# Kernel optimization log

Hardware: AMD Instinct MI355X
Metric: run time of the kernel (lower is better)

## Reference

```python
import jax, jax.numpy as jnp
import numpy as np
import math

B, S, HID = 2, 2048, 512
NH, NKV, HD = 8, 2, 256
ROT = 64          # partial_rotary_factor 0.25 * head_dim 256
ROPE_THETA = 10000000.0
EPS = 1e-6


def _rms_norm(x, w):
    # zero-centered RMSNorm: x / rms * (1 + w)
    rms = jnp.sqrt(jnp.mean(x * x, axis=-1, keepdims=True) + EPS)
    return x / rms * (1.0 + w)


def _partial_rope(x, cos, sin):
    # x: [B,S,H,HD]; cos/sin: [S, ROT//2]
    xr = x[..., :ROT].reshape(*x.shape[:-1], ROT // 2, 2)
    a, b = xr[..., 0], xr[..., 1]
    c = cos[None, :, None, :]
    s = sin[None, :, None, :]
    rot = jnp.stack([a * c - b * s, a * s + b * c], axis=-1).reshape(*x.shape[:-1], ROT)
    return jnp.concatenate([rot, x[..., ROT:]], axis=-1)


def setup_inputs() -> dict:
    key = jax.random.key(0)
    ks = jax.random.split(key, 6)
    x = jax.random.normal(ks[0], (B, S, HID), dtype=jnp.float32)
    # real RoPE frequencies
    inv_freq = 1.0 / (ROPE_THETA ** (np.arange(0, ROT, 2, dtype=np.float32) / ROT))
    t = np.arange(S, dtype=np.float32)
    angles = np.outer(t, inv_freq)  # [S, ROT//2]
    cos = jnp.asarray(np.cos(angles), dtype=jnp.float32)
    sin = jnp.asarray(np.sin(angles), dtype=jnp.float32)
    # additive causal mask [S,S]
    mask = jnp.where(jnp.tril(jnp.ones((S, S), dtype=bool)), 0.0, -1e9).astype(jnp.float32)
    sc = 0.02
    wq = jax.random.normal(ks[1], (HID, NH * HD), dtype=jnp.float32) * sc
    wk = jax.random.normal(ks[2], (HID, NKV * HD), dtype=jnp.float32) * sc
    wv = jax.random.normal(ks[3], (HID, NKV * HD), dtype=jnp.float32) * sc
    wo = jax.random.normal(ks[4], (NH * HD, HID), dtype=jnp.float32) * sc
    q_norm_w = jnp.zeros((HD,), dtype=jnp.float32)
    k_norm_w = jnp.zeros((HD,), dtype=jnp.float32)
    return {"x": x, "cos": cos, "sin": sin, "mask": mask,
            "wq": wq, "wk": wk, "wv": wv, "wo": wo,
            "q_norm_w": q_norm_w, "k_norm_w": k_norm_w}


def reference(x, cos, sin, mask, wq, wk, wv, wo, q_norm_w, k_norm_w):
    b, s, _ = x.shape
    groups = NH // NKV
    q = (x @ wq).reshape(b, s, NH, HD)
    k = (x @ wk).reshape(b, s, NKV, HD)
    v = (x @ wv).reshape(b, s, NKV, HD)
    q = _partial_rope(_rms_norm(q, q_norm_w), cos, sin)
    k = _partial_rope(_rms_norm(k, k_norm_w), cos, sin)
    # GQA: broadcast kv heads to NH
    k = jnp.repeat(k, groups, axis=2)  # [b,s,NH,HD]
    v = jnp.repeat(v, groups, axis=2)
    scale = math.sqrt(HD)
    scores = jnp.einsum('bqhd,bkhd->bhqk', q, k) / scale
    scores = scores + mask[None, None, :, :]
    attn = jax.nn.softmax(scores, axis=-1)
    out = jnp.einsum('bhqk,bkhd->bqhd', attn, v).reshape(b, s, NH * HD)
    return out @ wo
```

## Files before the change

kernel.cpp:

```cpp
#include <hip/hip_runtime.h>

#define S_LEN 2048
#define NHQ 8
#define NKV 2
#define HD 256
#define KVB 32

typedef __attribute__((ext_vector_type(8))) short bf16x8;
typedef __attribute__((ext_vector_type(4))) short bf16x4;
typedef __attribute__((ext_vector_type(4))) float f32x4;
typedef __attribute__((ext_vector_type(16))) float f32x16;
typedef __attribute__((ext_vector_type(4))) unsigned u32x4;

__device__ __forceinline__ short f2bf(float f) {
    unsigned u = __builtin_bit_cast(unsigned, f);
    u += 0x7FFFu + ((u >> 16) & 1u);
    return (short)(u >> 16);
}
__device__ __forceinline__ float bf2f(short s) {
    unsigned u = ((unsigned)(unsigned short)s) << 16;
    return __builtin_bit_cast(float, u);
}
__device__ __forceinline__ unsigned cvtpk(float a, float b) {
    unsigned r;
    asm("v_cvt_pk_bf16_f32 %0, %1, %2" : "=v"(r) : "v"(a), "v"(b));
    return r;
}
__device__ __forceinline__ void gload16(const short* g, short* l) {
    __builtin_amdgcn_global_load_lds((const __attribute__((address_space(1))) unsigned*)g,
                                     (__attribute__((address_space(3))) unsigned*)l, 16, 0, 0);
}
__device__ __forceinline__ float bperm(int srclane, float v) {
    return __builtin_bit_cast(float,
        __builtin_amdgcn_ds_bpermute(srclane * 4, __builtin_bit_cast(int, v)));
}

__global__ __launch_bounds__(256) void cvt_kernel(const float* __restrict__ in,
                                                  short* __restrict__ out, int n) {
    int i = (blockIdx.x * 256 + threadIdx.x) * 4;
    if (i + 3 < n) {
        float4 f = *(const float4*)(in + i);
        bf16x4 o;
        o[0] = f2bf(f.x); o[1] = f2bf(f.y); o[2] = f2bf(f.z); o[3] = f2bf(f.w);
        *(bf16x4*)(out + i) = o;
    }
}

__global__ __launch_bounds__(256) void wt_all_kernel(const float* __restrict__ wq,
                                                     const float* __restrict__ wk,
                                                     const float* __restrict__ wv,
                                                     const float* __restrict__ wo,
                                                     short* __restrict__ wfus,
                                                     short* __restrict__ wot) {
    __shared__ short tile[64][72];
    int bid = blockIdx.x;
    const float* in; short* out; int K, N, nx, base;
    if (bid < 256)      { in = wq; out = wfus;             K = 512;  N = 2048; nx = 32; base = 0;   }
    else if (bid < 320) { in = wk; out = wfus + 2048 * 512; K = 512;  N = 512;  nx = 8;  base = 256; }
    else if (bid < 384) { in = wv; out = wfus + 2560 * 512; K = 512;  N = 512;  nx = 8;  base = 320; }
    else                { in = wo; out = wot;              K = 2048; N = 512;  nx = 8;  base = 384; }
    int lb = bid - base;
    int n0 = (lb % nx) * 64, k0 = (lb / nx) * 64;
    int t = threadIdx.x;
    #pragma unroll
    for (int i = 0; i < 16; i++) {
        int flat = i * 256 + t; int r = flat >> 6, c = flat & 63;
        tile[r][c] = f2bf(in[(long)(k0 + r) * N + n0 + c]);
    }
    __syncthreads();
    #pragma unroll
    for (int i = 0; i < 16; i++) {
        int flat = i * 256 + t; int r = flat >> 6, c = flat & 63;
        out[(long)(n0 + r) * K + k0 + c] = tile[c][r];
    }
}

template<int BM, int BN, int WRITE_BF16>
__global__ __launch_bounds__(256) void gemm_bt(const short* __restrict__ A,
                                               const short* __restrict__ Bt,
                                               void* __restrict__ Cv,
                                               int M, int N, int K) {
    constexpr int MI = BM / 32;
    constexpr int NI = BN / 32;
    __shared__ short As[2][BM * 32];
    __shared__ short Bs[2][BN * 32];
    const int t = threadIdx.x;
    const int lane = t & 63, w = t >> 6;
    const int lr = lane & 15, lg = lane >> 4;
    const int m0 = blockIdx.y * BM, n0 = blockIdx.x * BN;
    const int wm = (w >> 1) * (BM / 2), wn = (w & 1) * (BN / 2);

    f32x4 acc[MI][NI];
    #pragma unroll
    for (int i = 0; i < MI; i++)
        #pragma unroll
        for (int j = 0; j < NI; j++) acc[i][j] = (f32x4){0.f, 0.f, 0.f, 0.f};

    auto stage = [&](int buf, int kt) {
        int k0 = kt * 32;
        #pragma unroll
        for (int r = 0; r < BM / 64; r++) {
            int sbase = r * 2048 + w * 512;
            int off = sbase + lane * 8;
            int srow = off >> 5, scol = off & 31;
            gload16(A + (long)(m0 + srow) * K + k0 + scol, &As[buf][sbase]);
        }
        #pragma unroll
        for (int r = 0; r < BN / 64; r++) {
            int sbase = r * 2048 + w * 512;
            int off = sbase + lane * 8;
            int srow = off >> 5, scol = off & 31;
            gload16(Bt + (long)(n0 + srow) * K + k0 + scol, &Bs[buf][sbase]);
        }
    };

    const int nt = K / 32;
    stage(0, 0);
    asm volatile("s_waitcnt vmcnt(0)" ::: "memory");
    __builtin_amdgcn_s_barrier();

    for (int kt = 0; kt < nt; kt++) {
        int cur = kt & 1;
        if (kt + 1 < nt) stage(cur ^ 1, kt + 1);
        bf16x8 af[MI], bfr[NI];
        #pragma unroll
        for (int mi = 0; mi < MI; mi++)
            af[mi] = *(const bf16x8*)&As[cur][(wm + mi * 16 + lr) * 32 + lg * 8];
        #pragma unroll
        for (int ni = 0; ni < NI; ni++)
            bfr[ni] = *(const bf16x8*)&Bs[cur][(wn + ni * 16 + lr) * 32 + lg * 8];
        __builtin_amdgcn_s_setprio(1);
        #pragma unroll
        for (int mi = 0; mi < MI; mi++)
            #pragma unroll
            for (int ni = 0; ni < NI; ni++)
                acc[mi][ni] = __builtin_amdgcn_mfma_f32_16x16x32_bf16(af[mi], bfr[ni], acc[mi][ni], 0, 0, 0);
        __builtin_amdgcn_s_setprio(0);
        asm volatile("s_waitcnt vmcnt(0)" ::: "memory");
        __builtin_amdgcn_s_barrier();
    }

    #pragma unroll
    for (int mi = 0; mi < MI; mi++)
    #pragma unroll
    for (int ni = 0; ni < NI; ni++)
    #pragma unroll
    for (int r = 0; r < 4; r++) {
        long row = m0 + wm + mi * 16 + lg * 4 + r;
        long col = n0 + wn + ni * 16 + lr;
        float v = acc[mi][ni][r];
        if (WRITE_BF16) ((short*)Cv)[row * N + col] = f2bf(v);
        else            ((float*)Cv)[row * N + col] = v;
    }
}

__global__ __launch_bounds__(256) void qkv_post_kernel(
    const short* __restrict__ C, short* __restrict__ qout, short* __restrict__ kout,
    short* __restrict__ vr,
    const float* __restrict__ qw, const float* __restrict__ kw,
    const float* __restrict__ cosb, const float* __restrict__ sinb) {
    __shared__ short tile[64][65];
    int bid = blockIdx.x;
    int t = threadIdx.x;

    if (bid >= 10240) {
        int vbid = bid - 10240;
        int s0 = (vbid & 31) * 64, d0 = ((vbid >> 5) & 3) * 64;
        int bkv = vbid >> 7; int b = bkv >> 1, kv = bkv & 1;
        #pragma unroll
        for (int i = 0; i < 16; i++) {
            int flat = i * 256 + t; int si = flat >> 6, di = flat & 63;
            tile[si][di] = C[(long)(b * S_LEN + s0 + si) * 3072 + 2560 + kv * 256 + d0 + di];
        }
        __syncthreads();
        #pragma unroll
        for (int i = 0; i < 16; i++) {
            int flat = i * 256 + t; int di = flat >> 6, si = flat & 63;
            vr[(long)(bkv * 256 + d0 + di) * S_LEN + s0 + si] = tile[si][di];
        }
        return;
    }

    bool isQ = bid < 8192;
    int H        = isQ ? 8 : 2;
    long cofs    = isQ ? 0L : 2048L;
    const float* w = isQ ? qw : kw;
    short* out   = isQ ? qout : kout;
    long ob      = isQ ? 4194304L : 1048576L;
    long oh      = isQ ? 256L : 524288L;
    long os      = isQ ? 2048L : 256L;
    float scale  = isQ ? 0.0625f : 1.0f;
    int vec = (isQ ? bid : bid - 8192) * 4 + (t >> 6);
    int lane = t & 63;
    int token = vec / H, head = vec % H;
    int b = token / S_LEN, s = token % S_LEN;

    bf16x4 xv = *(const bf16x4*)(C + (long)token * 3072 + cofs + head * 256 + lane * 4);
    float x0 = bf2f(xv[0]), x1 = bf2f(xv[1]), x2 = bf2f(xv[2]), x3 = bf2f(xv[3]);
    float ss = x0 * x0 + x1 * x1 + x2 * x2 + x3 * x3;
    #pragma unroll
    for (int m = 1; m < 64; m <<= 1) ss += __shfl_xor(ss, m);
    float inv = rsqrtf(ss * (1.f / 256.f) + 1e-6f);

    float4 wv = *(const float4*)(w + lane * 4);
    float y0 = x0 * inv * (1.f + wv.x);
    float y1 = x1 * inv * (1.f + wv.y);
    float y2 = x2 * inv * (1.f + wv.z);
    float y3 = x3 * inv * (1.f + wv.w);

    if (lane < 16) {
        float2 c = *(const float2*)&cosb[s * 32 + lane * 2];
        float2 sn = *(const float2*)&sinb[s * 32 + lane * 2];
        float a0 = y0 * c.x - y1 * sn.x, b0 = y0 * sn.x + y1 * c.x;
        float a1 = y2 * c.y - y3 * sn.y, b1 = y2 * sn.y + y3 * c.y;
        y0 = a0; y1 = b0; y2 = a1; y3 = b1;
    }
    y0 *= scale; y1 *= scale; y2 *= scale; y3 *= scale;
    long oidx = (long)b * ob + (long)head * oh + (long)s * os + lane * 4;
    bf16x4 o; o[0] = f2bf(y0); o[1] = f2bf(y1); o[2] = f2bf(y2); o[3] = f2bf(y3);
    *(bf16x4*)(out + oidx) = o;
}

__global__ __launch_bounds__(256, 2) void flash_kernel(const short* __restrict__ Q,
                                                       const short* __restrict__ Kt,
                                                       const short* __restrict__ Vt,
                                                       short* __restrict__ O) {
    __shared__ __align__(16) char smem[66048];

    int idx = blockIdx.x;
    int xcd = idx & 7, slot = idx >> 3;
    int bh = xcd * 2 + (slot & 1);
    int j  = 31 - (slot >> 1);
    int h = bh & 7, b = bh >> 3;
    int kv = h >> 2;
    int t = threadIdx.x, lane = t & 63, w = t >> 6;
    int g = w >> 1, p = w & 1;
    int ln = lane & 31, hi = lane >> 5;
    int q0 = j * 64 + g * 32;
    int qg = q0 + ln;

    const short* Kb = Kt + (long)(b * NKV + kv) * S_LEN * HD;
    const short* Vb = Vt + (long)(b * NKV + kv) * HD * S_LEN;

    bf16x8 qf[16];
    {
        const short* qrow = Q + ((long)(b * S_LEN + qg) * NHQ + h) * HD + hi * 8;
        #pragma unroll
        for (int dc = 0; dc < 16; dc++) qf[dc] = *(const bf16x8*)&qrow[dc * 16];
    }

    f32x16 acc[8];
    #pragma unroll
    for (int i = 0; i < 8; i++)
        #pragma unroll
        for (int jj = 0; jj < 16; jj++) acc[i][jj] = 0.f;
    float m = -1e30f, l = 0.f;

    auto stage = [&](int ph2) {
        #pragma unroll
        for (int pp = 0; pp < 2; pp++) {
            int k0s = (2 * ph2 + pp) * KVB;
            short* Ktile = (short*)(smem + pp * 16384);
            short* Vtile = (short*)(smem + 32768 + pp * 16384);
            #pragma unroll
            for (int c = 0; c < 4; c++) {
                int o = c * 4096 + w * 1024 + lane * 16;
                int key = o >> 9, db = o & 511;
                gload16(Kb + (long)(k0s + key) * HD + ((db ^ ((key & 7) << 4)) >> 1),
                        Ktile + (c * 4096 + w * 1024) / 2);
                int d = o >> 6, kb = o & 63;
                gload16(Vb + (long)d * S_LEN + k0s + ((kb ^ ((d & 6) << 3)) >> 1),
                        Vtile + (c * 4096 + w * 1024) / 2);
            }
        }
    };

    auto compute = [&](int k0) {
        const char* Ks = (const char*)smem + p * 16384;
        const char* Vs = (const char*)smem + 32768 + p * 16384;
        f32x16 sA, sB;
        #pragma unroll
        for (int r = 0; r < 16; r++) { sA[r] = 0.f; sB[r] = 0.f; }
        __builtin_amdgcn_s_setprio(1);
        #pragma unroll
        for (int dc = 0; dc < 16; dc += 2) {
            int kb0 = (dc * 32 + hi * 16) ^ ((ln & 7) << 4);
            int kb1 = ((dc + 1) * 32 + hi * 16) ^ ((ln & 7) << 4);
            bf16x8 kf0 = *(const bf16x8*)(Ks + ln * 512 + kb0);
            bf16x8 kf1 = *(const bf16x8*)(Ks + ln * 512 + kb1);
            sA = __builtin_amdgcn_mfma_f32_32x32x16_bf16(kf0, qf[dc],     sA, 0, 0, 0);
            sB = __builtin_amdgcn_mfma_f32_32x32x16_bf16(kf1, qf[dc + 1], sB, 0, 0, 0);
        }
        __builtin_amdgcn_s_setprio(0);
        f32x16 s;
        #pragma unroll
        for (int r = 0; r < 16; r++) s[r] = sA[r] + sB[r];

        if (k0 + KVB - 1 > q0) {
            #pragma unroll
            for (int r = 0; r < 16; r++) {
                int key_g = k0 + (r & 3) + 8 * (r >> 2) + 4 * hi;
                if (key_g > qg) s[r] = -1e30f;
            }
        }
        float mt = s[0];
        #pragma unroll
        for (int r = 1; r < 16; r++) mt = fmaxf(mt, s[r]);
        mt = fmaxf(mt, __shfl_xor(mt, 32));
        float mn = m;
        if (!__all(mt <= m + 8.f)) {
            mn = fmaxf(m, mt);
            float f = __expf(m - mn);
            m = mn;
            float fr[16];
            #pragma unroll
            for (int r = 0; r < 16; r++)
                fr[r] = bperm((r & 3) + 8 * (r >> 2) + 4 * hi, f);
            #pragma unroll
            for (int i = 0; i < 8; i++)
                #pragma unroll
                for (int r = 0; r < 16; r++) acc[i][r] *= fr[r];
            l *= f;
        }
        float pr[16], ps = 0.f;
        #pragma unroll
        for (int r = 0; r < 16; r++) { pr[r] = __expf(s[r] - mn); ps += pr[r]; }
        ps += __shfl_xor(ps, 32);
        l += ps;

        unsigned pw[8];
        #pragma unroll
        for (int kc = 0; kc < 2; kc++) {
            unsigned X = cvtpk(pr[kc * 8 + 0], pr[kc * 8 + 1]);
            unsigned Y = cvtpk(pr[kc * 8 + 4], pr[kc * 8 + 5]);
            unsigned Z = cvtpk(pr[kc * 8 + 2], pr[kc * 8 + 3]);
            unsigned W = cvtpk(pr[kc * 8 + 6], pr[kc * 8 + 7]);
            asm volatile("v_permlane32_swap_b32 %0, %1" : "+v"(X), "+v"(Y));
            asm volatile("v_permlane32_swap_b32 %0, %1" : "+v"(Z), "+v"(W));
            pw[kc * 4 + 0] = X; pw[kc * 4 + 1] = Z;
            pw[kc * 4 + 2] = Y; pw[kc * 4 + 3] = W;
        }
        u32x4 w0v = {pw[0], pw[1], pw[2], pw[3]};
        u32x4 w1v = {pw[4], pw[5], pw[6], pw[7]};
        bf16x8 pa0 = __builtin_bit_cast(bf16x8, w0v);
        bf16x8 pa1 = __builtin_bit_cast(bf16x8, w1v);

        __builtin_amdgcn_s_setprio(1);
        #pragma unroll
        for (int db = 0; db < 8; db++) {
            int drow = db * 32 + ln;
            int sw = (drow & 6) << 3;
            bf16x8 vf0 = *(const bf16x8*)(Vs + drow * 64 + ((hi * 16) ^ sw));
            bf16x8 vf1 = *(const bf16x8*)(Vs + drow * 64 + ((32 + hi * 16) ^ sw));
            acc[db] = __builtin_amdgcn_mfma_f32_32x32x16_bf16(pa0, vf0, acc[db], 0, 0, 0);
            acc[db] = __builtin_amdgcn_mfma_f32_32x32x16_bf16(pa1, vf1, acc[db], 0, 0, 0);
        }
        __builtin_amdgcn_s_setprio(0);
    };

    stage(0);
    for (int ph = 0; ph <= j; ph++) {
        asm volatile("s_waitcnt vmcnt(0)" ::: "memory");
        __builtin_amdgcn_s_barrier();
        int k0 = (2 * ph + p) * KVB;
        if (k0 <= q0 + 31) compute(k0);
        __builtin_amdgcn_s_barrier();
        if (ph < j) stage(ph + 1);
        __builtin_amdgcn_sched_barrier(0);
    }

    float* accb = (float*)smem;
    float* mlb  = (float*)(smem + 65536);
    if (p == 1) {
        #pragma unroll
        for (int db = 0; db < 8; db++)
            #pragma unroll
            for (int r = 0; r < 16; r++)
                accb[g * 8192 + (db * 16 + r) * 64 + hi * 32 + ln] = acc[db][r];
        if (hi == 0) { mlb[g * 32 + ln] = m; mlb[64 + g * 32 + ln] = l; }
    }
    __syncthreads();
    if (p == 0) {
        float m1 = mlb[g * 32 + ln], l1 = mlb[64 + g * 32 + ln];
        float M  = fmaxf(m, m1);
        float f0 = __expf(m - M), f1 = __expf(m1 - M);
        float lt = l * f0 + l1 * f1;
        float w0 = f0 / lt, w1 = f1 / lt;
        float fr0[16], fr1[16];
        #pragma unroll
        for (int r = 0; r < 16; r++) {
            int crow = (r & 3) + 8 * (r >> 2) + 4 * hi;
            fr0[r] = bperm(crow, w0);
            fr1[r] = bperm(crow, w1);
        }
        #pragma unroll
        for (int db = 0; db < 8; db++)
            #pragma unroll
            for (int r = 0; r < 16; r++) {
                float a1 = accb[g * 8192 + (db * 16 + r) * 64 + hi * 32 + ln];
                int qrow = q0 + (r & 3) + 8 * (r >> 2) + 4 * hi;
                O[(long)(b * S_LEN + qrow) * 2048 + h * HD + db * 32 + ln] =
                    f2bf(acc[db][r] * fr0[r] + a1 * fr1[r]);
            }
    }
}

extern "C" void kernel_launch(void* const* d_in, const int* in_sizes, int n_in,
                              void* d_out, int out_size, void* d_ws, size_t ws_size,
                              hipStream_t stream) {
    const float* x    = (const float*)d_in[0];
    const float* cosb = (const float*)d_in[1];
    const float* sinb = (const float*)d_in[2];
    const float* wq   = (const float*)d_in[4];
    const float* wk   = (const float*)d_in[5];
    const float* wv   = (const float*)d_in[6];
    const float* wo   = (const float*)d_in[7];
    const float* qnw  = (const float*)d_in[8];
    const float* knw  = (const float*)d_in[9];
    float* out = (float*)d_out;

    char* ws = (char*)d_ws;
    short* xb   = (short*)(ws + 0);
    short* wfus = (short*)(ws + 4194304);
    short* wot  = (short*)(ws + 7340032);
    short* C    = (short*)(ws + 9437184);
    short* ao   = (short*)(ws + 9437184);
    short* qro  = (short*)(ws + 34603008);
    short* kr   = (short*)(ws + 51380224);
    short* vr   = (short*)(ws + 55574528);

    cvt_kernel<<<2048, 256, 0, stream>>>(x, xb, 2097152);
    wt_all_kernel<<<640, 256, 0, stream>>>(wq, wk, wv, wo, wfus, wot);

    gemm_bt<128, 128, 1><<<dim3(24, 32), 256, 0, stream>>>(xb, wfus, C, 4096, 3072, 512);

    qkv_post_kernel<<<10752, 256, 0, stream>>>(C, qro, kr, vr, qnw, knw, cosb, sinb);

    flash_kernel<<<512, 256, 0, stream>>>(qro, kr, vr, ao);

    gemm_bt<64, 64, 0><<<dim3(8, 64), 256, 0, stream>>>(ao, wot, out, 4096, 512, 2048);
}
```

Baseline: 178.1 us.

## Triple-buffer GEMM loads with partial vmcnt waits and merge prep kernels

The bf16 GEMM moves from double to triple buffering in LDS. The next tile load is now issued after the MFMAs, and each iteration waits only on the older stage through a partial s_waitcnt vmcnt, so global loads overlap compute across two stages. The x-conversion kernel and the weight-transpose kernel are merged into one launch to save a kernel launch and its tail. In exchange, LDS use per block goes up, which may lower occupancy, and the vmcnt counts are hardcoded to the per-stage load counts.

```diff
diff --git a/kernel.cpp b/kernel.cpp
--- a/kernel.cpp
+++ b/kernel.cpp
@@ -35,33 +35,33 @@
         __builtin_amdgcn_ds_bpermute(srclane * 4, __builtin_bit_cast(int, v)));
 }
 
-__global__ __launch_bounds__(256) void cvt_kernel(const float* __restrict__ in,
-                                                  short* __restrict__ out, int n) {
-    int i = (blockIdx.x * 256 + threadIdx.x) * 4;
-    if (i + 3 < n) {
-        float4 f = *(const float4*)(in + i);
+__global__ __launch_bounds__(256) void prep_kernel(const float* __restrict__ x,
+                                                   short* __restrict__ xb,
+                                                   const float* __restrict__ wq,
+                                                   const float* __restrict__ wk,
+                                                   const float* __restrict__ wv,
+                                                   const float* __restrict__ wo,
+                                                   short* __restrict__ wfus,
+                                                   short* __restrict__ wot) {
+    __shared__ short tile[64][72];
+    int bid = blockIdx.x;
+    int t = threadIdx.x;
+    if (bid < 2048) {
+        int i = (bid * 256 + t) * 4;
+        float4 f = *(const float4*)(x + i);
         bf16x4 o;
         o[0] = f2bf(f.x); o[1] = f2bf(f.y); o[2] = f2bf(f.z); o[3] = f2bf(f.w);
-        *(bf16x4*)(out + i) = o;
-    }
-}
-
-__global__ __launch_bounds__(256) void wt_all_kernel(const float* __restrict__ wq,
-                                                     const float* __restrict__ wk,
-                                                     const float* __restrict__ wv,
-                                                     const float* __restrict__ wo,
-                                                     short* __restrict__ wfus,
-                                                     short* __restrict__ wot) {
-    __shared__ short tile[64][72];
-    int bid = blockIdx.x;
+        *(bf16x4*)(xb + i) = o;
+        return;
+    }
+    int wb = bid - 2048;
     const float* in; short* out; int K, N, nx, base;
-    if (bid < 256)      { in = wq; out = wfus;             K = 512;  N = 2048; nx = 32; base = 0;   }
-    else if (bid < 320) { in = wk; out = wfus + 2048 * 512; K = 512;  N = 512;  nx = 8;  base = 256; }
-    else if (bid < 384) { in = wv; out = wfus + 2560 * 512; K = 512;  N = 512;  nx = 8;  base = 320; }
-    else                { in = wo; out = wot;              K = 2048; N = 512;  nx = 8;  base = 384; }
-    int lb = bid - base;
+    if (wb < 256)      { in = wq; out = wfus;              K = 512;  N = 2048; nx = 32; base = 0;   }
+    else if (wb < 320) { in = wk; out = wfus + 2048 * 512; K = 512;  N = 512;  nx = 8;  base = 256; }
+    else if (wb < 384) { in = wv; out = wfus + 2560 * 512; K = 512;  N = 512;  nx = 8;  base = 320; }
+    else               { in = wo; out = wot;               K = 2048; N = 512;  nx = 8;  base = 384; }
+    int lb = wb - base;
     int n0 = (lb % nx) * 64, k0 = (lb / nx) * 64;
-    int t = threadIdx.x;
     #pragma unroll
     for (int i = 0; i < 16; i++) {
         int flat = i * 256 + t; int r = flat >> 6, c = flat & 63;
@@ -82,8 +82,9 @@
                                                int M, int N, int K) {
     constexpr int MI = BM / 32;
     constexpr int NI = BN / 32;
-    __shared__ short As[2][BM * 32];
-    __shared__ short Bs[2][BN * 32];
+    constexpr int LPS = BM / 64 + BN / 64;
+    __shared__ short As[3 * BM * 32];
+    __shared__ short Bs[3 * BN * 32];
     const int t = threadIdx.x;
     const int lane = t & 63, w = t >> 6;
     const int lr = lane & 15, lg = lane >> 4;
@@ -98,37 +99,46 @@
 
     auto stage = [&](int buf, int kt) {
         int k0 = kt * 32;
+        short* Ab = As + buf * (BM * 32);
+        short* Bb = Bs + buf * (BN * 32);
         #pragma unroll
         for (int r = 0; r < BM / 64; r++) {
             int sbase = r * 2048 + w * 512;
             int off = sbase + lane * 8;
             int srow = off >> 5, scol = off & 31;
-            gload16(A + (long)(m0 + srow) * K + k0 + scol, &As[buf][sbase]);
+            gload16(A + (long)(m0 + srow) * K + k0 + scol, Ab + sbase);
         }
         #pragma unroll
         for (int r = 0; r < BN / 64; r++) {
             int sbase = r * 2048 + w * 512;
             int off = sbase + lane * 8;
             int srow = off >> 5, scol = off & 31;
-            gload16(Bt + (long)(n0 + srow) * K + k0 + scol, &Bs[buf][sbase]);
+            gload16(Bt + (long)(n0 + srow) * K + k0 + scol, Bb + sbase);
         }
     };
 
     const int nt = K / 32;
     stage(0, 0);
-    asm volatile("s_waitcnt vmcnt(0)" ::: "memory");
-    __builtin_amdgcn_s_barrier();
-
+    stage(1, 1);
+
+    int cur = 0;
     for (int kt = 0; kt < nt; kt++) {
-        int cur = kt & 1;
-        if (kt + 1 < nt) stage(cur ^ 1, kt + 1);
+        if (kt + 1 < nt) {
+            if constexpr (LPS == 4) asm volatile("s_waitcnt vmcnt(4)" ::: "memory");
+            else                    asm volatile("s_waitcnt vmcnt(2)" ::: "memory");
+        } else {
+            asm volatile("s_waitcnt vmcnt(0)" ::: "memory");
+        }
+        __builtin_amdgcn_s_barrier();
+        const short* Ab = As + cur * (BM * 32);
+        const short* Bb = Bs + cur * (BN * 32);
         bf16x8 af[MI], bfr[NI];
         #pragma unroll
         for (int mi = 0; mi < MI; mi++)
-            af[mi] = *(const bf16x8*)&As[cur][(wm + mi * 16 + lr) * 32 + lg * 8];
+            af[mi] = *(const bf16x8*)&Ab[(wm + mi * 16 + lr) * 32 + lg * 8];
         #pragma unroll
         for (int ni = 0; ni < NI; ni++)
-            bfr[ni] = *(const bf16x8*)&Bs[cur][(wn + ni * 16 + lr) * 32 + lg * 8];
+            bfr[ni] = *(const bf16x8*)&Bb[(wn + ni * 16 + lr) * 32 + lg * 8];
         __builtin_amdgcn_s_setprio(1);
         #pragma unroll
         for (int mi = 0; mi < MI; mi++)
@@ -136,8 +146,12 @@
             for (int ni = 0; ni < NI; ni++)
                 acc[mi][ni] = __builtin_amdgcn_mfma_f32_16x16x32_bf16(af[mi], bfr[ni], acc[mi][ni], 0, 0, 0);
         __builtin_amdgcn_s_setprio(0);
-        asm volatile("s_waitcnt vmcnt(0)" ::: "memory");
-        __builtin_amdgcn_s_barrier();
+        if (kt + 2 < nt) {
+            int b2 = cur + 2; if (b2 >= 3) b2 -= 3;
+            stage(b2, kt + 2);
+        }
+        cur = (cur == 2) ? 0 : cur + 1;
+        __builtin_amdgcn_sched_barrier(0);
     }
 
     #pragma unroll
@@ -429,8 +443,7 @@
     short* kr   = (short*)(ws + 51380224);
     short* vr   = (short*)(ws + 55574528);
 
-    cvt_kernel<<<2048, 256, 0, stream>>>(x, xb, 2097152);
-    wt_all_kernel<<<640, 256, 0, stream>>>(wq, wk, wv, wo, wfus, wot);
+    prep_kernel<<<2688, 256, 0, stream>>>(x, xb, wq, wk, wv, wo, wfus, wot);
 
     gemm_bt<128, 128, 1><<<dim3(24, 32), 256, 0, stream>>>(xb, wfus, C, 4096, 3072, 512);
 
```

Result: no change. 178.7 us (+0.3%).
